# Optimization experiments

Measured on AMD Instinct MI355X. Metric: run time of the kernel, lower is better.

The kernel has to match this reference:

```python
import jax, jax.numpy as jnp
import numpy as np

B, I, H = 16384, 512, 512


def setup_inputs() -> dict:
    key = jax.random.key(0)
    ks = jax.random.split(key, 10)
    inputs = jax.random.normal(ks[0], (B, I), dtype=jnp.float32)
    state = jax.random.normal(ks[1], (B, 2 * H), dtype=jnp.float32)
    # xavier_uniform for w_ih: U(-a, a), a = sqrt(6 / (fan_in + fan_out))
    a = float(np.sqrt(6.0 / (2 * H + I)))
    w_ih = jax.random.uniform(ks[2], (2 * H, I), jnp.float32, -a, a)
    b_h = jnp.zeros((H,), jnp.float32)
    pi = float(np.pi)
    d1 = jax.random.uniform(ks[3], (H,), jnp.float32, -pi, pi)
    d2 = jax.random.uniform(ks[4], (H,), jnp.float32, -pi, pi)
    d3 = jax.random.uniform(ks[5], (H,), jnp.float32, -pi, pi)
    re1 = jax.random.uniform(ks[6], (H,), jnp.float32, -1.0, 1.0)
    im1 = jax.random.uniform(ks[7], (H,), jnp.float32, -1.0, 1.0)
    re2 = jax.random.uniform(ks[8], (H,), jnp.float32, -1.0, 1.0)
    im2 = jax.random.uniform(ks[9], (H,), jnp.float32, -1.0, 1.0)
    perm = jnp.asarray(np.random.default_rng(0).permutation(H), dtype=jnp.int32)
    return {"inputs": inputs, "state": state, "w_ih": w_ih, "b_h": b_h,
            "d1": d1, "d2": d2, "d3": d3,
            "re1": re1, "im1": im1, "re2": re2, "im2": im2, "perm": perm}


def _diag_mul(w, z):
    # multiply by exp(i*w) built as complex(cos w, sin w), as in the original
    return jax.lax.complex(jnp.cos(w), jnp.sin(w)) * z


def _reflect(re, im, z):
    # z - (2/||v||^2) * (z @ conj(v)) outer v   (faithful to original matmuls)
    v = jax.lax.complex(re, im)                 # [H]
    vz = z @ jnp.conj(v)                        # [B]
    factor = 2.0 / jnp.sum(re * re + im * im)   # real scalar
    return z - factor * vz[:, None] * v[None, :]


def _modrelu(z, b):
    norm = jnp.abs(z)
    scale = jax.nn.relu(norm + b) / (norm + 1e-6)
    return z * scale


def reference(inputs, state, w_ih, b_h, d1, d2, d3, re1, im1, re2, im2, perm):
    inputs_mul = inputs @ w_ih.T                                  # [B, 2H]
    z_in = jax.lax.complex(inputs_mul[:, :H], inputs_mul[:, H:])  # [B, H] c64
    state_c = jax.lax.complex(state[:, :H], state[:, H:])
    # Unitary chain (computed in original forward, but its result `preact` is
    # never used for the returned state -- faithfully reproduced).
    s = _diag_mul(d1, state_c)
    s = jnp.fft.fft(s, axis=-1)
    s = _reflect(re1, im1, s)
    s = s[:, perm]                 # column permutation (z.T[P].T)
    s = _diag_mul(d2, s)
    s = jnp.fft.ifft(s, axis=-1)
    s = _reflect(re2, im2, s)
    s = _diag_mul(d3, s)
    preact = z_in + s              # dead in original; kept for fidelity
    new_state_c = _modrelu(z_in, b_h)
    return jnp.concatenate([jnp.real(new_state_c), jnp.imag(new_state_c)], axis=1)
```

## Files before the change

### kernel.cpp

```cpp
#include <hip/hip_runtime.h>
#include <hip/hip_bf16.h>


typedef __attribute__((ext_vector_type(8))) short bf16x8;
typedef __attribute__((ext_vector_type(4))) float f32x4;

#define BM 128
#define BK 64
#define KDIM 512
#define NDIM 1024
#define NKT 8

#define VMCNT(n) asm volatile("s_waitcnt vmcnt(" #n ")" ::: "memory")
#define LGKM(n)  asm volatile("s_waitcnt lgkmcnt(" #n ")" ::: "memory")

__device__ __forceinline__ unsigned short f2bf(float f) {
    unsigned u = __builtin_bit_cast(unsigned, f);
    u += 0x7fffu + ((u >> 16) & 1u);
    return (unsigned short)(u >> 16);
}

__global__ __launch_bounds__(256) void cvt_both(
    const float* __restrict__ A, const float* __restrict__ W,
    unsigned short* __restrict__ Abf, unsigned short* __restrict__ Wbf,
    int nA4, int nTot4) {
    int i = blockIdx.x * blockDim.x + threadIdx.x;
    int stride = gridDim.x * blockDim.x;
    for (; i < nTot4; i += stride) {
        float4 v;
        if (i < nA4) v = reinterpret_cast<const float4*>(A)[i];
        else         v = reinterpret_cast<const float4*>(W)[i - nA4];
        ushort4 o;
        o.x = f2bf(v.x); o.y = f2bf(v.y); o.z = f2bf(v.z); o.w = f2bf(v.w);
        if (i < nA4) reinterpret_cast<ushort4*>(Abf)[i] = o;
        else         reinterpret_cast<ushort4*>(Wbf)[i - nA4] = o;
    }
}

__device__ __forceinline__ void gload_lds16(const void* g, void* l) {
    __builtin_amdgcn_global_load_lds(
        (const __attribute__((address_space(1))) unsigned int*)g,
        (__attribute__((address_space(3))) unsigned int*)l, 16, 0, 0);
}

__global__ __launch_bounds__(256, 2) void gemm_modrelu(
    const unsigned short* __restrict__ A,
    const unsigned short* __restrict__ W,
    const float* __restrict__ bh,
    float* __restrict__ out)
{
    __shared__ __align__(16) char smem[65536];
    unsigned short* At0 = (unsigned short*)smem;
    unsigned short* Bt0 = (unsigned short*)(smem + 32768);
    float* C = (float*)smem;

    const int tid = threadIdx.x;
    const int w   = tid >> 6;
    const int l   = tid & 63;
    const int l15 = l & 15;
    const int l4  = l >> 4;
    const int wm  = w >> 1;
    const int wn  = w & 1;

    const int bx = blockIdx.x;
    const int lg = (bx & 7) * 128 + (bx >> 3);
    const int mb = lg >> 3;
    const int cb = lg & 7;

    const int srow = l >> 3;
    const int sseg = (l & 7) ^ srow;
    const unsigned short* ga[4];
    const unsigned short* gb[4];
    int ldso[4];
#pragma unroll
    for (int is = 0; is < 4; ++is) {
        int row  = w * 32 + is * 8 + srow;
        ga[is]   = A + (size_t)(mb * BM + row) * KDIM + sseg * 8;
        int wrow = (row >> 6) * 512 + cb * 64 + (row & 63);
        gb[is]   = W + (size_t)wrow * KDIM + sseg * 8;
        ldso[is] = (w * 32 + is * 8) * BK;
    }

    auto stage = [&](int kt, int buf) {
        unsigned short* at = At0 + buf * (BM * BK);
        unsigned short* bt = Bt0 + buf * (BM * BK);
#pragma unroll
        for (int is = 0; is < 4; ++is)
            gload_lds16(ga[is] + kt * BK, at + ldso[is]);
#pragma unroll
        for (int is = 0; is < 4; ++is)
            gload_lds16(gb[is] + kt * BK, bt + ldso[is]);
    };

    f32x4 acc[4][4];
#pragma unroll
    for (int i = 0; i < 4; ++i)
#pragma unroll
        for (int j = 0; j < 4; ++j) acc[i][j] = f32x4{0.f, 0.f, 0.f, 0.f};

    stage(0, 0);
    stage(1, 1);
    VMCNT(8);
    __builtin_amdgcn_s_barrier();

#pragma unroll
    for (int kt = 0; kt < NKT; ++kt) {
        const int buf = kt & 1;
        const unsigned short* at = At0 + buf * (BM * BK);
        const unsigned short* bt = Bt0 + buf * (BM * BK);

#pragma unroll
        for (int ks = 0; ks < 2; ++ks) {
            bf16x8 af[4], bf[4];
#pragma unroll
            for (int i = 0; i < 4; ++i) {
                int row = wm * 64 + i * 16 + l15;
                af[i] = *(const bf16x8*)(&at[row * BK + (((ks * 4 + l4) ^ (row & 7)) * 8)]);
            }
#pragma unroll
            for (int j = 0; j < 4; ++j) {
                int row = (j >> 1) * 64 + wn * 32 + (j & 1) * 16 + l15;
                bf[j] = *(const bf16x8*)(&bt[row * BK + (((ks * 4 + l4) ^ (row & 7)) * 8)]);
            }
            LGKM(0);
            __builtin_amdgcn_sched_barrier(0);
            __builtin_amdgcn_s_setprio(1);
#pragma unroll
            for (int i = 0; i < 4; ++i)
#pragma unroll
                for (int j = 0; j < 4; ++j)
                    acc[i][j] = __builtin_amdgcn_mfma_f32_16x16x32_bf16(
                        af[i], bf[j], acc[i][j], 0, 0, 0);
            __builtin_amdgcn_s_setprio(0);
        }

        if (kt + 1 < NKT) {
            __builtin_amdgcn_s_barrier();
            if (kt + 2 < NKT) {
                stage(kt + 2, buf);
                VMCNT(8);
            } else {
                VMCNT(0);
            }
            __builtin_amdgcn_s_barrier();
        }
    }

    __syncthreads();
#pragma unroll
    for (int j = 0; j < 2; ++j) {
        int col = wn * 32 + j * 16 + l15;
        float b = bh[cb * 64 + col];
#pragma unroll
        for (int i = 0; i < 4; ++i) {
#pragma unroll
            for (int jj = 0; jj < 4; ++jj) {
                int rowl = wm * 64 + i * 16 + l4 * 4 + jj;
                float re  = acc[i][j][jj];
                float imv = acc[i][j + 2][jj];
                float norm  = sqrtf(re * re + imv * imv);
                float scale = fmaxf(norm + b, 0.f) * __builtin_amdgcn_rcpf(norm + 1e-6f);
                C[rowl * 128 + col]      = re  * scale;
                C[rowl * 128 + 64 + col] = imv * scale;
            }
        }
    }
    __syncthreads();

    const int seg   = l & 31;
    const int rhalf = l >> 5;
#pragma unroll
    for (int it = 0; it < 16; ++it) {
        int rowl = w * 32 + it * 2 + rhalf;
        f32x4 v = *reinterpret_cast<const f32x4*>(&C[rowl * 128 + seg * 4]);
        size_t m = (size_t)(mb * BM + rowl);
        int n = (seg < 16) ? (cb * 64 + seg * 4)
                           : (512 + cb * 64 + (seg - 16) * 4);
        *reinterpret_cast<f32x4*>(out + m * NDIM + n) = v;
    }
}

extern "C" void kernel_launch(void* const* d_in, const int* in_sizes, int n_in,
                              void* d_out, int out_size, void* d_ws, size_t ws_size,
                              hipStream_t stream) {
    const float* inputs = (const float*)d_in[0];
    const float* w_ih   = (const float*)d_in[2];
    const float* b_h    = (const float*)d_in[3];
    float* out = (float*)d_out;

    unsigned short* Abf = (unsigned short*)d_ws;
    unsigned short* Wbf = (unsigned short*)((char*)d_ws + (size_t)16384 * 512 * 2);

    const int nA4 = (16384 * 512) / 4;
    const int nW4 = (1024 * 512) / 4;
    cvt_both<<<2048, 256, 0, stream>>>(inputs, w_ih, Abf, Wbf, nA4, nA4 + nW4);

    gemm_modrelu<<<1024, 256, 0, stream>>>(Abf, Wbf, b_h, out);
}
```

Measured before the change: 42.64 us.

## Halve K tile to shrink LDS, raise occupancy, and store epilogue directly

Cuts the K tile from 64 to 32, so the double-buffered LDS footprint drops from 64KB to 32KB. Launch bounds move to 4 blocks per CU for more latency hiding, and the XOR swizzle is reworked for the narrower rows. The epilogue no longer stages results through LDS for coalesced float4 stores; each lane writes its scalars straight to global memory. The risks are twice as many barrier/sync iterations, possible register pressure under the higher occupancy target, and uncoalesced 4-byte global stores.

```diff
diff --git a/kernel.cpp b/kernel.cpp
--- a/kernel.cpp
+++ b/kernel.cpp
@@ -6,10 +6,10 @@
 typedef __attribute__((ext_vector_type(4))) float f32x4;
 
 #define BM 128
-#define BK 64
+#define BK 32
 #define KDIM 512
 #define NDIM 1024
-#define NKT 8
+#define NKT 16
 
 #define VMCNT(n) asm volatile("s_waitcnt vmcnt(" #n ")" ::: "memory")
 #define LGKM(n)  asm volatile("s_waitcnt lgkmcnt(" #n ")" ::: "memory")
@@ -43,16 +43,14 @@
         (__attribute__((address_space(3))) unsigned int*)l, 16, 0, 0);
 }
 
-__global__ __launch_bounds__(256, 2) void gemm_modrelu(
+__global__ __launch_bounds__(256, 4) void gemm_modrelu(
     const unsigned short* __restrict__ A,
     const unsigned short* __restrict__ W,
     const float* __restrict__ bh,
     float* __restrict__ out)
 {
-    __shared__ __align__(16) char smem[65536];
-    unsigned short* At0 = (unsigned short*)smem;
-    unsigned short* Bt0 = (unsigned short*)(smem + 32768);
-    float* C = (float*)smem;
+    __shared__ __align__(16) unsigned short At0[2][BM * BK];
+    __shared__ __align__(16) unsigned short Bt0[2][BM * BK];
 
     const int tid = threadIdx.x;
     const int w   = tid >> 6;
@@ -67,29 +65,27 @@
     const int mb = lg >> 3;
     const int cb = lg & 7;
 
-    const int srow = l >> 3;
-    const int sseg = (l & 7) ^ srow;
-    const unsigned short* ga[4];
-    const unsigned short* gb[4];
-    int ldso[4];
+    const int srow = l >> 2;
+    const int sseg = (l & 3) ^ ((l >> 3) & 3);
+    const unsigned short* ga[2];
+    const unsigned short* gb[2];
+    int ldso[2];
 #pragma unroll
-    for (int is = 0; is < 4; ++is) {
-        int row  = w * 32 + is * 8 + srow;
+    for (int is = 0; is < 2; ++is) {
+        int row  = w * 32 + is * 16 + srow;
         ga[is]   = A + (size_t)(mb * BM + row) * KDIM + sseg * 8;
         int wrow = (row >> 6) * 512 + cb * 64 + (row & 63);
         gb[is]   = W + (size_t)wrow * KDIM + sseg * 8;
-        ldso[is] = (w * 32 + is * 8) * BK;
+        ldso[is] = (w * 32 + is * 16) * BK;
     }
 
     auto stage = [&](int kt, int buf) {
-        unsigned short* at = At0 + buf * (BM * BK);
-        unsigned short* bt = Bt0 + buf * (BM * BK);
 #pragma unroll
-        for (int is = 0; is < 4; ++is)
-            gload_lds16(ga[is] + kt * BK, at + ldso[is]);
+        for (int is = 0; is < 2; ++is)
+            gload_lds16(ga[is] + kt * BK, &At0[buf][ldso[is]]);
 #pragma unroll
-        for (int is = 0; is < 4; ++is)
-            gload_lds16(gb[is] + kt * BK, bt + ldso[is]);
+        for (int is = 0; is < 2; ++is)
+            gload_lds16(gb[is] + kt * BK, &Bt0[buf][ldso[is]]);
     };
 
     f32x4 acc[4][4];
@@ -100,45 +96,42 @@
 
     stage(0, 0);
     stage(1, 1);
-    VMCNT(8);
+    VMCNT(4);
     __builtin_amdgcn_s_barrier();
+
+    const int rslot = (l4 ^ ((l15 >> 1) & 3)) * 8;
 
 #pragma unroll
     for (int kt = 0; kt < NKT; ++kt) {
         const int buf = kt & 1;
-        const unsigned short* at = At0 + buf * (BM * BK);
-        const unsigned short* bt = Bt0 + buf * (BM * BK);
 
+        bf16x8 af[4], bfr[4];
 #pragma unroll
-        for (int ks = 0; ks < 2; ++ks) {
-            bf16x8 af[4], bf[4];
+        for (int i = 0; i < 4; ++i) {
+            int row = wm * 64 + i * 16 + l15;
+            af[i] = *(const bf16x8*)(&At0[buf][row * BK + rslot]);
+        }
 #pragma unroll
-            for (int i = 0; i < 4; ++i) {
-                int row = wm * 64 + i * 16 + l15;
-                af[i] = *(const bf16x8*)(&at[row * BK + (((ks * 4 + l4) ^ (row & 7)) * 8)]);
-            }
+        for (int j = 0; j < 4; ++j) {
+            int row = (j >> 1) * 64 + wn * 32 + (j & 1) * 16 + l15;
+            bfr[j] = *(const bf16x8*)(&Bt0[buf][row * BK + rslot]);
+        }
+        LGKM(0);
+        __builtin_amdgcn_sched_barrier(0);
+        __builtin_amdgcn_s_setprio(1);
 #pragma unroll
-            for (int j = 0; j < 4; ++j) {
-                int row = (j >> 1) * 64 + wn * 32 + (j & 1) * 16 + l15;
-                bf[j] = *(const bf16x8*)(&bt[row * BK + (((ks * 4 + l4) ^ (row & 7)) * 8)]);
-            }
-            LGKM(0);
-            __builtin_amdgcn_sched_barrier(0);
-            __builtin_amdgcn_s_setprio(1);
+        for (int i = 0; i < 4; ++i)
 #pragma unroll
-            for (int i = 0; i < 4; ++i)
-#pragma unroll
-                for (int j = 0; j < 4; ++j)
-                    acc[i][j] = __builtin_amdgcn_mfma_f32_16x16x32_bf16(
-                        af[i], bf[j], acc[i][j], 0, 0, 0);
-            __builtin_amdgcn_s_setprio(0);
-        }
+            for (int j = 0; j < 4; ++j)
+                acc[i][j] = __builtin_amdgcn_mfma_f32_16x16x32_bf16(
+                    af[i], bfr[j], acc[i][j], 0, 0, 0);
+        __builtin_amdgcn_s_setprio(0);
 
         if (kt + 1 < NKT) {
             __builtin_amdgcn_s_barrier();
             if (kt + 2 < NKT) {
                 stage(kt + 2, buf);
-                VMCNT(8);
+                VMCNT(4);
             } else {
                 VMCNT(0);
             }
@@ -146,37 +139,24 @@
         }
     }
 
-    __syncthreads();
 #pragma unroll
     for (int j = 0; j < 2; ++j) {
-        int col = wn * 32 + j * 16 + l15;
-        float b = bh[cb * 64 + col];
+        int n = cb * 64 + wn * 32 + j * 16 + l15;
+        float b = bh[n];
 #pragma unroll
         for (int i = 0; i < 4; ++i) {
 #pragma unroll
             for (int jj = 0; jj < 4; ++jj) {
-                int rowl = wm * 64 + i * 16 + l4 * 4 + jj;
+                int m = mb * BM + wm * 64 + i * 16 + l4 * 4 + jj;
                 float re  = acc[i][j][jj];
                 float imv = acc[i][j + 2][jj];
                 float norm  = sqrtf(re * re + imv * imv);
                 float scale = fmaxf(norm + b, 0.f) * __builtin_amdgcn_rcpf(norm + 1e-6f);
-                C[rowl * 128 + col]      = re  * scale;
-                C[rowl * 128 + 64 + col] = imv * scale;
+                float* po = out + (size_t)m * NDIM + n;
+                po[0]   = re  * scale;
+                po[512] = imv * scale;
             }
         }
-    }
-    __syncthreads();
-
-    const int seg   = l & 31;
-    const int rhalf = l >> 5;
-#pragma unroll
-    for (int it = 0; it < 16; ++it) {
-        int rowl = w * 32 + it * 2 + rhalf;
-        f32x4 v = *reinterpret_cast<const f32x4*>(&C[rowl * 128 + seg * 4]);
-        size_t m = (size_t)(mb * BM + rowl);
-        int n = (seg < 16) ? (cb * 64 + seg * 4)
-                           : (512 + cb * 64 + (seg - 16) * 4);
-        *reinterpret_cast<f32x4*>(out + m * NDIM + n) = v;
     }
 }
 
```

Measured after the change: 43.75 us. 1.03x slower.
